# Kernel tuning notes

Hardware: AMD Instinct MI355X
Metric: run time of the kernel (lower is better)

The kernel has to match this reference:

```python
import jax, jax.numpy as jnp
import numpy as np

N = 100000          # num nodes
E = 1600000         # num edges (before self loops)
IN_C = 128
OUT_C = 64
RATIO = 0.5
NEG_SLOPE = 0.2


def setup_inputs() -> dict:
    key = jax.random.key(0)
    k1, k2, k3, k4, k5 = jax.random.split(key, 5)
    x = jax.random.normal(k1, (N, IN_C), jnp.float32)
    # edges with no self loops (module removes then re-adds self loops)
    src = jax.random.randint(k2, (E,), 0, N, dtype=jnp.int32)
    off = jax.random.randint(k3, (E,), 1, N, dtype=jnp.int32)
    tgt = (src + off) % N
    edge_index = jnp.stack([src, tgt])  # [2, E], row0=source(j), row1=target(i)
    # glorot init
    s_w = float(np.sqrt(6.0 / (IN_C + OUT_C)))
    weight = jax.random.uniform(k4, (IN_C, OUT_C), jnp.float32, -s_w, s_w)
    s_a = float(np.sqrt(6.0 / (1 + 2 * OUT_C)))
    att = jax.random.uniform(k5, (1, 2 * OUT_C), jnp.float32, -s_a, s_a)
    batch = jnp.zeros((N,), jnp.int32)  # single graph
    return {"x": x, "weight": weight, "att": att,
            "edge_index": edge_index, "batch": batch, "bn": 0}


def reference(x, weight, att, edge_index, batch, bn):
    # add self loops (static shapes: E + N edges)
    loops = jnp.arange(N, dtype=edge_index.dtype)
    src = jnp.concatenate([edge_index[0], loops])  # edge_index_j (source)
    tgt = jnp.concatenate([edge_index[1], loops])  # edge_index_i (target)

    h = x @ weight                      # [N, OUT_C]
    x_j = h[src]                        # [E+N, OUT_C] gathered source feats
    x_i = h[tgt]

    # alpha = (cat([x_i, x_j]) * att).sum(-1)
    alpha = x_i @ att[0, :OUT_C] + x_j @ att[0, OUT_C:]   # [E+N]
    alpha = jnp.where(alpha > 0, alpha, NEG_SLOPE * alpha)  # leaky_relu

    # edge-softmax grouped by target node (every node has a self loop -> no empty segment)
    m = jax.ops.segment_max(alpha, tgt, num_segments=N)
    a = jnp.exp(alpha - m[tgt])
    denom = jax.ops.segment_sum(a, tgt, num_segments=N)
    alpha = a / (denom[tgt] + 1e-16)

    # node importance = sum of attention over outgoing edges (grouped by source)
    alpha_sum = jax.ops.segment_sum(alpha, src, num_segments=N)

    # topk node selection (ratio of all nodes; single graph)
    k = int(np.ceil(RATIO * N))
    _, topk_idx = jax.lax.top_k(alpha_sum, k)
    node_mask = jnp.zeros((N,), bool).at[topk_idx].set(True)

    # filter_dn: keep edges whose both endpoints survive; mask instead of compacting
    edge_mask = node_mask[src] & node_mask[tgt]
    alpha_m = jnp.where(edge_mask, alpha, 0.0)

    # weighted scatter-add aggregation to target nodes (aggr='add')
    out = jax.ops.segment_sum(alpha_m[:, None] * x_j, tgt, num_segments=N)  # [N, OUT_C]
    # bn flag is 0 -> BatchNorm skipped
    return out, edge_mask, node_mask
```

## Files before the change

kernel.cpp:

```cpp
#include <hip/hip_runtime.h>
#include <stdint.h>

#define IN_C 128
#define OUT_C 64
#define NEG_SLOPE 0.2f
#define RB 256
#define RBINS 512
#define STAGE 8192
#define NGH (RBINS * RB)
#define NGHS (RBINS * RBINS)
#define KC 8
#define SXW 192

typedef unsigned int u32;
typedef unsigned long long u64;

__device__ __forceinline__ u32 fenc(float f) {
  u32 u = __float_as_uint(f);
  return (u & 0x80000000u) ? ~u : (u | 0x80000000u);
}
__device__ __forceinline__ u64 key64(float v, int i) {
  return (((u64)fenc(v)) << 32) | (u64)(0xffffffffu - (u32)i);
}

__global__ __launch_bounds__(128) void k_gemm(const float* __restrict__ x,
                                              const float* __restrict__ w,
                                              const float* __restrict__ att,
                                              float* __restrict__ h,
                                              float* __restrict__ ai, float* __restrict__ aj,
                                              int N) {
  __shared__ float sw[IN_C * OUT_C];
  __shared__ float sx[KC * SXW];
  int tid = threadIdx.x;
  int rbase = blockIdx.x * 128;

  for (int i = tid; i < (IN_C * OUT_C) / 4; i += 128)
    ((float4*)sw)[i] = ((const float4*)w)[i];

  int c0 = (tid & 7) * 8;
  int rg = tid >> 3;
  int sxbase = rg * 12;
  float acc[8][8];
#pragma unroll
  for (int i = 0; i < 8; i++)
#pragma unroll
    for (int j = 0; j < 8; j++) acc[i][j] = 0.f;

  int grow = rbase + tid;
  int base = (tid >> 3) * 12 + (tid & 7);
  const float* xp = &x[(size_t)grow * IN_C];

  float4 pv0 = make_float4(0.f, 0.f, 0.f, 0.f);
  float4 pv1 = make_float4(0.f, 0.f, 0.f, 0.f);
  if (grow < N) {
    pv0 = *(const float4*)&xp[0];
    pv1 = *(const float4*)&xp[4];
  }

  for (int kb = 0; kb < IN_C; kb += KC) {
    __syncthreads();
    sx[0 * SXW + base] = pv0.x;
    sx[1 * SXW + base] = pv0.y;
    sx[2 * SXW + base] = pv0.z;
    sx[3 * SXW + base] = pv0.w;
    sx[4 * SXW + base] = pv1.x;
    sx[5 * SXW + base] = pv1.y;
    sx[6 * SXW + base] = pv1.z;
    sx[7 * SXW + base] = pv1.w;
    if (kb + KC < IN_C && grow < N) {
      pv0 = *(const float4*)&xp[kb + KC];
      pv1 = *(const float4*)&xp[kb + KC + 4];
    }
    __syncthreads();
#pragma unroll
    for (int kl = 0; kl < KC; ++kl) {
      int kg = kb + kl;
      float xr[8], wv[8];
      *(float4*)&xr[0] = *(const float4*)&sx[kl * SXW + sxbase];
      *(float4*)&xr[4] = *(const float4*)&sx[kl * SXW + sxbase + 4];
      *(float4*)&wv[0] = *(const float4*)&sw[kg * OUT_C + c0];
      *(float4*)&wv[4] = *(const float4*)&sw[kg * OUT_C + c0 + 4];
#pragma unroll
      for (int i = 0; i < 8; ++i)
#pragma unroll
        for (int j = 0; j < 8; ++j)
          acc[i][j] += xr[i] * wv[j];
    }
  }

  float pi[8], pj[8];
#pragma unroll
  for (int i = 0; i < 8; ++i) { pi[i] = 0.f; pj[i] = 0.f; }
#pragma unroll
  for (int j = 0; j < 8; ++j) {
    float a0 = att[c0 + j], a1 = att[OUT_C + c0 + j];
#pragma unroll
    for (int i = 0; i < 8; ++i) {
      pi[i] += acc[i][j] * a0;
      pj[i] += acc[i][j] * a1;
    }
  }
#pragma unroll
  for (int o = 1; o < 8; o <<= 1) {
#pragma unroll
    for (int i = 0; i < 8; ++i) {
      pi[i] += __shfl_xor(pi[i], o);
      pj[i] += __shfl_xor(pj[i], o);
    }
  }
#pragma unroll
  for (int i = 0; i < 8; ++i) {
    int row = rbase + rg * 8 + i;
    if (row < N) {
      *(float4*)&h[(size_t)row * OUT_C + c0]     = make_float4(acc[i][0], acc[i][1], acc[i][2], acc[i][3]);
      *(float4*)&h[(size_t)row * OUT_C + c0 + 4] = make_float4(acc[i][4], acc[i][5], acc[i][6], acc[i][7]);
      if ((tid & 7) == 0) { ai[row] = pi[i]; aj[row] = pj[i]; }
    }
  }
}

__global__ __launch_bounds__(256) void k_rhist_t(const int* __restrict__ tgt,
                                                 int E, int EN, int chunk, u32* __restrict__ gh,
                                                 u32* __restrict__ hist8, u32* __restrict__ done,
                                                 u32* __restrict__ sel, u32* __restrict__ cnt, u32 k) {
  __shared__ u32 lh[RBINS];
  int tid = threadIdx.x, b = blockIdx.x;
  if (b == 0) {
    for (int i = tid; i < 2048; i += 256) hist8[i] = 0u;
    if (tid < 8) { done[tid] = 0u; cnt[tid] = 0u; }
    if (tid == 0) { sel[0] = 0u; sel[1] = 0u; sel[2] = k; sel[3] = 0u; }
  }
  for (int d = tid; d < RBINS; d += 256) lh[d] = 0u;
  __syncthreads();
  int lo = b * chunk, hi = min(lo + chunk, EN);
  for (int e = lo + tid; e < hi; e += 256) {
    int t = (e < E) ? tgt[e] : e - E;
    atomicAdd(&lh[((u32)t) >> 8], 1u);
  }
  __syncthreads();
  for (int d = tid; d < RBINS; d += 256) gh[d * RB + b] = lh[d];
}

__global__ __launch_bounds__(256) void k_scanA(const u32* __restrict__ in, u32* __restrict__ out,
                                               u32* __restrict__ bsum, int n) {
  __shared__ u32 s[256];
  int i = blockIdx.x * 256 + threadIdx.x;
  u32 v = (i < n) ? in[i] : 0u;
  s[threadIdx.x] = v;
  __syncthreads();
  for (int o = 1; o < 256; o <<= 1) {
    u32 t = (threadIdx.x >= (unsigned)o) ? s[threadIdx.x - o] : 0u;
    __syncthreads();
    s[threadIdx.x] += t;
    __syncthreads();
  }
  if (i < n) out[i] = s[threadIdx.x] - v;
  if (threadIdx.x == 255) bsum[blockIdx.x] = s[255];
}

__global__ __launch_bounds__(1024) void k_scanB(u32* __restrict__ bsum, int nb) {
  __shared__ u32 s[1024];
  int tid = threadIdx.x;
  u32 v = (tid < nb) ? bsum[tid] : 0u;
  s[tid] = v;
  __syncthreads();
  for (int o = 1; o < 1024; o <<= 1) {
    u32 t = (tid >= o) ? s[tid - o] : 0u;
    __syncthreads();
    s[tid] += t;
    __syncthreads();
  }
  if (tid < nb) bsum[tid] = s[tid] - v;
}

__global__ __launch_bounds__(256) void k_scanC(u32* __restrict__ out, const u32* __restrict__ bsum, int n) {
  int i = blockIdx.x * 256 + threadIdx.x;
  if (i < n) out[i] += bsum[blockIdx.x];
}

__global__ __launch_bounds__(256) void k_rscatter_t(const int* __restrict__ src, const int* __restrict__ tgt,
                                                    int E, int EN, int chunk,
                                                    const u32* __restrict__ gh, u32* __restrict__ bufB) {
  __shared__ u32 cnt[RBINS];
  int tid = threadIdx.x, b = blockIdx.x;
  for (int d = tid; d < RBINS; d += 256) cnt[d] = gh[d * RB + b];
  __syncthreads();
  int lo = b * chunk, hi = min(lo + chunk, EN);
  for (int e = lo + tid; e < hi; e += 256) {
    int s, t;
    if (e < E) { s = src[e]; t = tgt[e]; } else { s = t = e - E; }
    u32 p = atomicAdd(&cnt[((u32)t) >> 8], 1u);
    bufB[p] = (((u32)t & 255u) << 24) | (u32)s;
  }
}

__global__ __launch_bounds__(256) void k_rpass2(const u32* __restrict__ in, u32* __restrict__ out,
                                                const u32* __restrict__ gh, u32* __restrict__ ghs,
                                                u32* __restrict__ offT,
                                                const float* __restrict__ ai, const float* __restrict__ aj,
                                                float* __restrict__ alpha,
                                                int N, int EN) {
  __shared__ u32 hist[256];
  __shared__ u32 sc[256];
  __shared__ u32 lhs[RBINS];
  __shared__ u32 stage[STAGE];
  int tid = threadIdx.x, d = blockIdx.x;
  u32 start = gh[d * RB];
  u32 end = (d < RBINS - 1) ? gh[(d + 1) * RB] : (u32)EN;
  int sz = (int)(end - start);
  hist[tid] = 0u;
  for (int dd = tid; dd < RBINS; dd += 256) lhs[dd] = 0u;
  __syncthreads();
  for (u32 p = start + tid; p < end; p += 256) {
    u32 it = in[p];
    atomicAdd(&hist[it >> 24], 1u);
    atomicAdd(&lhs[(it & 0xffffffu) >> 8], 1u);
  }
  __syncthreads();
  for (int dd = tid; dd < RBINS; dd += 256) ghs[dd * RBINS + d] = lhs[dd];
  u32 hv = hist[tid];
  sc[tid] = hv;
  __syncthreads();
  for (int o = 1; o < 256; o <<= 1) {
    u32 t = (tid >= o) ? sc[tid - o] : 0u;
    __syncthreads();
    sc[tid] += t;
    __syncthreads();
  }
  u32 excl = sc[tid] - hv;
  int node = (d << 8) + tid;
  if (node < N) offT[node] = start + excl;
  if (node == 0) offT[N] = (u32)EN;
  hist[tid] = excl;
  __syncthreads();
  bool staged = (sz <= STAGE);
  for (u32 p = start + tid; p < end; p += 256) {
    u32 it = in[p];
    u32 lp = atomicAdd(&hist[it >> 24], 1u);
    if (staged) stage[lp] = it;
    else out[start + lp] = it;
  }
  __syncthreads();
  if (staged)
    for (int i = tid; i < sz; i += 256) out[start + i] = stage[i];
  __syncthreads();
  if (node < N) {
    int lb = (tid > 0) ? (int)sc[tid - 1] : 0;
    int le = (int)sc[tid];
    float an = ai[node];
    float mx = -1e30f;
    for (int i = lb; i < le; ++i) {
      u32 it = staged ? stage[i] : out[start + i];
      float a = an + aj[it & 0xffffffu];
      a = a > 0.f ? a : NEG_SLOPE * a;
      mx = fmaxf(mx, a);
      if (staged) stage[i] = __float_as_uint(a);
    }
    float sm = 0.f;
    for (int i = lb; i < le; ++i) {
      float a;
      if (staged) a = __uint_as_float(stage[i]);
      else {
        u32 it = out[start + i];
        a = an + aj[it & 0xffffffu];
        a = a > 0.f ? a : NEG_SLOPE * a;
      }
      float v = expf(a - mx);
      sm += v;
      if (staged) stage[i] = __float_as_uint(v);
      else alpha[start + i] = v;
    }
    float inv = 1.f / (sm + 1e-16f);
    for (int i = lb; i < le; ++i) {
      float v = staged ? __uint_as_float(stage[i]) : alpha[start + i];
      alpha[start + i] = v * inv;
    }
  }
}

__global__ __launch_bounds__(256) void k_rscatter_s(const u32* __restrict__ csr,
                                                    const float* __restrict__ alpha,
                                                    const u32* __restrict__ gh, const u32* __restrict__ ghs,
                                                    u64* __restrict__ bufB, int EN) {
  __shared__ u32 cnt[RBINS];
  int tid = threadIdx.x, d = blockIdx.x;
  for (int dd = tid; dd < RBINS; dd += 256) cnt[dd] = ghs[dd * RBINS + d];
  __syncthreads();
  u32 start = gh[d * RB];
  u32 end = (d < RBINS - 1) ? gh[(d + 1) * RB] : (u32)EN;
  for (u32 e = start + tid; e < end; e += 256) {
    u32 s = csr[e] & 0xffffffu;
    u32 p = atomicAdd(&cnt[s >> 8], 1u);
    bufB[p] = (((u64)(s & 255u)) << 32) | __float_as_uint(alpha[e]);
  }
}

__global__ __launch_bounds__(256) void k_asum_acc(const u64* __restrict__ bufB,
                                                  const u32* __restrict__ ghs,
                                                  float* __restrict__ asum,
                                                  u32* __restrict__ hist8, u32* __restrict__ done,
                                                  u32* __restrict__ sel,
                                                  int N, int EN, int nblk) {
  __shared__ float sums[256];
  __shared__ u32 lh[256];
  __shared__ u32 s[256];
  __shared__ u32 sres;
  int tid = threadIdx.x, d = blockIdx.x;
  u32 start = ghs[d * RBINS];
  u32 end = (d < RBINS - 1) ? ghs[(d + 1) * RBINS] : (u32)EN;
  sums[tid] = 0.f;
  __syncthreads();
  for (u32 p = start + tid; p < end; p += 256) {
    u64 it = bufB[p];
    atomicAdd(&sums[(u32)(it >> 32)], __uint_as_float((u32)it));
  }
  __syncthreads();
  int node = d * 256 + tid;
  u32 bin = 256u;
  if (node < N) {
    float v = sums[tid];
    asum[node] = v;
    bin = (u32)(key64(v, node) >> 56) & 255u;
  }
  lh[tid] = 0u;
  __syncthreads();
  if (bin < 256u) atomicAdd(&lh[bin], 1u);
  __syncthreads();
  if (lh[tid]) atomicAdd(&hist8[tid], lh[tid]);
  __syncthreads();
  if (tid == 0)
    sres = __hip_atomic_fetch_add(&done[0], 1u, __ATOMIC_ACQ_REL, __HIP_MEMORY_SCOPE_AGENT);
  __syncthreads();
  if (sres == (u32)(nblk - 1)) {
    u32 krem = sel[2];
    u32 hv = __hip_atomic_load(&hist8[255 - tid], __ATOMIC_RELAXED, __HIP_MEMORY_SCOPE_AGENT);
    s[tid] = hv;
    __syncthreads();
    for (int o = 1; o < 256; o <<= 1) {
      u32 t = (tid >= o) ? s[tid - o] : 0u;
      __syncthreads();
      s[tid] += t;
      __syncthreads();
    }
    u32 cum = s[tid], prev = (tid > 0) ? s[tid - 1] : 0u;
    if (cum >= krem && prev < krem) {
      int dsel = 255 - tid;
      ((u64*)sel)[0] = (u64)(u32)dsel;
      sel[2] = krem - prev;
    }
  }
}

__global__ __launch_bounds__(256) void k_histpick(const float* __restrict__ asum,
                                                  const u32* __restrict__ list_in, const u32* __restrict__ cnt_in,
                                                  u32* __restrict__ list_out, u32* __restrict__ cnt_out,
                                                  u32* __restrict__ hist8, u32* __restrict__ done,
                                                  u32* __restrict__ sel, int N, int pass, int nblk) {
  __shared__ u32 lh[256];
  __shared__ u32 sres;
  __shared__ u32 s[256];
  int tid = threadIdx.x;
  lh[tid] = 0u;
  __syncthreads();
  u64 prefix = ((const u64*)sel)[0];
  int shift = 56 - 8 * pass;
  int n = list_in ? (int)*cnt_in : N;
  int i = blockIdx.x * 256 + tid;
  if (i < n) {
    int idx = list_in ? (int)list_in[i] : i;
    u64 k = key64(asum[idx], idx);
    bool ok = (pass == 0) || ((k >> (shift + 8)) == prefix);
    if (ok) {
      atomicAdd(&lh[(u32)(k >> shift) & 255u], 1u);
      if (list_out) {
        u32 p = atomicAdd(cnt_out, 1u);
        list_out[p] = (u32)idx;
      }
    }
  }
  __syncthreads();
  if (lh[tid]) atomicAdd(&hist8[pass * 256 + tid], lh[tid]);
  __syncthreads();
  if (tid == 0)
    sres = __hip_atomic_fetch_add(&done[pass], 1u, __ATOMIC_ACQ_REL, __HIP_MEMORY_SCOPE_AGENT);
  __syncthreads();
  if (sres == (u32)(nblk - 1)) {
    u32 krem = sel[2];
    u32 hv = __hip_atomic_load(&hist8[pass * 256 + (255 - tid)], __ATOMIC_RELAXED,
                               __HIP_MEMORY_SCOPE_AGENT);
    s[tid] = hv;
    __syncthreads();
    for (int o = 1; o < 256; o <<= 1) {
      u32 t = (tid >= o) ? s[tid - o] : 0u;
      __syncthreads();
      s[tid] += t;
      __syncthreads();
    }
    u32 cum = s[tid], prev = (tid > 0) ? s[tid - 1] : 0u;
    if (cum >= krem && prev < krem) {
      int dsel = 255 - tid;
      ((u64*)sel)[0] = (prefix << 8) | (u64)(u32)dsel;
      sel[2] = krem - prev;
    }
  }
}

__global__ __launch_bounds__(256) void k_finish(const float* __restrict__ asum,
                                                const u32* __restrict__ list, const u32* __restrict__ cntp,
                                                u32* __restrict__ sel) {
  __shared__ u64 keys[2048];
  __shared__ u32 cc;
  int tid = threadIdx.x;
  if (tid == 0) cc = 0u;
  __syncthreads();
  int n = (int)*cntp;
  u32 fsel = (u32)((const u64*)sel)[0];
  u32 krem = sel[2];
  for (int i = tid; i < n; i += 256) {
    int idx = (int)list[i];
    u64 k = key64(asum[idx], idx);
    if ((u32)(k >> 32) == fsel) {
      u32 p = atomicAdd(&cc, 1u);
      if (p < 2048) keys[p] = k;
    }
  }
  __syncthreads();
  int C = (int)min(cc, 2048u);
  for (int i = tid; i < C; i += 256) {
    u64 k = keys[i];
    u32 rank = 0;
    for (int j = 0; j < C; ++j)
      if (keys[j] > k) rank++;
    if (rank == krem - 1) ((u64*)sel)[0] = k;
  }
}

__global__ __launch_bounds__(256) void k_node_mask(const float* __restrict__ asum,
                                                   const u32* __restrict__ sel,
                                                   u32* __restrict__ nm,
                                                   float* __restrict__ out_node, int N) {
  int i = blockIdx.x * 256 + threadIdx.x;
  if (i >= N) return;
  u64 T = ((const u64*)sel)[0];
  bool m = key64(asum[i], i) >= T;
  nm[i] = m ? 1u : 0u;
  out_node[i] = m ? 1.f : 0.f;
}

__global__ __launch_bounds__(256) void k_mask(const int* __restrict__ src, const int* __restrict__ tgt,
                                              const u32* __restrict__ nm,
                                              float* __restrict__ out_edge,
                                              int E, int EN) {
  int e = blockIdx.x * 256 + threadIdx.x;
  if (e >= EN) return;
  int s, t;
  if (e < E) { s = src[e]; t = tgt[e]; } else { s = t = e - E; }
  out_edge[e] = (nm[s] && nm[t]) ? 1.f : 0.f;
}

__global__ __launch_bounds__(256) void k_aggregate(const u32* __restrict__ off,
                                                   const u32* __restrict__ csr,
                                                   const float* __restrict__ alpha,
                                                   const float* __restrict__ h,
                                                   const u32* __restrict__ nm,
                                                   float* __restrict__ out, int N) {
  int node = blockIdx.x * 4 + (threadIdx.x >> 6);
  int lane = threadIdx.x & 63;
  int g = lane >> 4;
  int c = lane & 15;
  if (node >= N) return;
  float4 acc = make_float4(0.f, 0.f, 0.f, 0.f);
  if (nm[node]) {
    u32 b = off[node], e2 = off[node + 1];
    for (u32 p0 = b; p0 < e2; p0 += 16) {
      float av[4];
      u32 sv[4];
#pragma unroll
      for (int q = 0; q < 4; ++q) {
        u32 p = p0 + q * 4 + (u32)g;
        bool ok = p < e2;
        u32 pp = ok ? p : b;
        u32 sp = csr[pp] & 0xffffffu;
        float a = alpha[pp];
        sv[q] = sp;
        av[q] = (ok && nm[sp]) ? a : 0.f;
      }
      float4 hv[4];
#pragma unroll
      for (int q = 0; q < 4; ++q) {
        hv[q] = make_float4(0.f, 0.f, 0.f, 0.f);
        if (av[q] != 0.f)
          hv[q] = *(const float4*)&h[(size_t)sv[q] * OUT_C + c * 4];
      }
#pragma unroll
      for (int q = 0; q < 4; ++q) {
        acc.x += av[q] * hv[q].x;
        acc.y += av[q] * hv[q].y;
        acc.z += av[q] * hv[q].z;
        acc.w += av[q] * hv[q].w;
      }
    }
#pragma unroll
    for (int o = 16; o < 64; o <<= 1) {
      acc.x += __shfl_xor(acc.x, o);
      acc.y += __shfl_xor(acc.y, o);
      acc.z += __shfl_xor(acc.z, o);
      acc.w += __shfl_xor(acc.w, o);
    }
  }
  if (g == 0)
    *(float4*)&out[(size_t)node * OUT_C + c * 4] = acc;
}

extern "C" void kernel_launch(void* const* d_in, const int* in_sizes, int n_in,
                              void* d_out, int out_size, void* d_ws, size_t ws_size,
                              hipStream_t stream) {
  const float* x   = (const float*)d_in[0];
  const float* w   = (const float*)d_in[1];
  const float* att = (const float*)d_in[2];
  const int*   ei  = (const int*)d_in[3];

  int N = in_sizes[0] / IN_C;
  int E = in_sizes[3] / 2;
  int EN = E + N;
  const int* src = ei;
  const int* tgt = ei + E;

  float* out      = (float*)d_out;
  float* out_edge = out + (size_t)N * OUT_C;
  float* out_node = out_edge + (size_t)EN;

  char* p = (char*)d_ws;
  auto alloc = [&](size_t bytes) -> char* {
    char* r = p;
    p += (bytes + 255) & ~(size_t)255;
    return r;
  };
  float* h     = (float*)alloc((size_t)N * OUT_C * 4);
  float* ai    = (float*)alloc((size_t)N * 4);
  float* aj    = (float*)alloc((size_t)N * 4);
  u32*   bufA  = (u32*)alloc((size_t)EN * 4);
  u64*   bufB  = (u64*)alloc((size_t)EN * 8);
  float* alpha = (float*)alloc((size_t)EN * 4);
  u32*   offT  = (u32*)alloc((size_t)(N + 1) * 4);
  u32*   gh    = (u32*)alloc((size_t)NGH * 4);
  u32*   ghs   = (u32*)alloc((size_t)NGHS * 4);
  u32*   bsum  = (u32*)alloc(2048 * 4);
  float* asum  = (float*)alloc((size_t)N * 4);
  u32*   nm    = (u32*)alloc((size_t)N * 4);
  u32*   hist8 = (u32*)alloc(2048 * 4);
  u32*   done  = (u32*)alloc(8 * 4);
  u32*   cnt   = (u32*)alloc(8 * 4);
  u32*   sel   = (u32*)alloc(256);
  u32*   listA = (u32*)alloc((size_t)N * 4);
  u32*   listB = (u32*)alloc((size_t)N * 4);

  u32 kSel = (u32)((N + 1) / 2);
  int chunk = (EN + RB - 1) / RB;
  int nScanT = (NGH + 255) / 256;
  int nScanS = (NGHS + 255) / 256;
  int gGemm = (N + 127) / 128;
  int gN = (N + 255) / 256;
  int gE = (EN + 255) / 256;
  int gNode4 = (N + 3) / 4;

  k_gemm<<<gGemm, 128, 0, stream>>>(x, w, att, h, ai, aj, N);

  k_rhist_t<<<RB, 256, 0, stream>>>(tgt, E, EN, chunk, gh, hist8, done, sel, cnt, kSel);
  k_scanA<<<nScanT, 256, 0, stream>>>(gh, gh, bsum, NGH);
  k_scanB<<<1, 1024, 0, stream>>>(bsum, nScanT);
  k_scanC<<<nScanT, 256, 0, stream>>>(gh, bsum, NGH);
  k_rscatter_t<<<RB, 256, 0, stream>>>(src, tgt, E, EN, chunk, gh, (u32*)bufB);
  k_rpass2<<<RBINS, 256, 0, stream>>>((u32*)bufB, bufA, gh, ghs, offT, ai, aj, alpha, N, EN);

  k_scanA<<<nScanS, 256, 0, stream>>>(ghs, ghs, bsum, NGHS);
  k_scanB<<<1, 1024, 0, stream>>>(bsum, nScanS);
  k_scanC<<<nScanS, 256, 0, stream>>>(ghs, bsum, NGHS);
  k_rscatter_s<<<RBINS, 256, 0, stream>>>(bufA, alpha, gh, ghs, bufB, EN);
  k_asum_acc<<<RBINS, 256, 0, stream>>>(bufB, ghs, asum, hist8, done, sel, N, EN, RBINS);

  k_histpick<<<gN, 256, 0, stream>>>(asum, nullptr, nullptr, listA, &cnt[1],
                                     hist8, done, sel, N, 1, gN);
  k_histpick<<<gN, 256, 0, stream>>>(asum, listA, &cnt[1], listB, &cnt[2],
                                     hist8, done, sel, N, 2, gN);
  k_histpick<<<gN, 256, 0, stream>>>(asum, listB, &cnt[2], listA, &cnt[3],
                                     hist8, done, sel, N, 3, gN);
  k_finish<<<1, 256, 0, stream>>>(asum, listA, &cnt[3], sel);

  k_node_mask<<<gN, 256, 0, stream>>>(asum, sel, nm, out_node, N);
  k_mask<<<gE, 256, 0, stream>>>(src, tgt, nm, out_edge, E, EN);
  k_aggregate<<<gNode4, 256, 0, stream>>>(offT, bufA, alpha, h, nm, out, N);
}
```

Measured before the change: 362.4 us.

## Replace scan-based radix partitions with fixed-capacity bucket slots and fewer top-k passes

```diff
diff --git a/kernel.cpp b/kernel.cpp
--- a/kernel.cpp
+++ b/kernel.cpp
@@ -7,12 +7,13 @@
 #define RB 256
 #define RBINS 512
 #define STAGE 8192
-#define NGH (RBINS * RB)
-#define NGHS (RBINS * RBINS)
+#define SCAP 5120
+#define SGRID (RBINS * SCAP)
 #define KC 8
 #define SXW 192
 
 typedef unsigned int u32;
+typedef unsigned char u8;
 typedef unsigned long long u64;
 
 __device__ __forceinline__ u32 fenc(float f) {
@@ -119,17 +120,14 @@
   }
 }
 
-__global__ __launch_bounds__(256) void k_rhist_t(const int* __restrict__ tgt,
-                                                 int E, int EN, int chunk, u32* __restrict__ gh,
-                                                 u32* __restrict__ hist8, u32* __restrict__ done,
-                                                 u32* __restrict__ sel, u32* __restrict__ cnt, u32 k) {
+__global__ __launch_bounds__(256) void k_part_t(const int* __restrict__ src, const int* __restrict__ tgt,
+                                                int E, int EN, int chunk,
+                                                u32* __restrict__ gcurT, u32* __restrict__ bufS,
+                                                u32* __restrict__ sel, u32 kSel) {
   __shared__ u32 lh[RBINS];
+  __shared__ u32 cur[RBINS];
   int tid = threadIdx.x, b = blockIdx.x;
-  if (b == 0) {
-    for (int i = tid; i < 2048; i += 256) hist8[i] = 0u;
-    if (tid < 8) { done[tid] = 0u; cnt[tid] = 0u; }
-    if (tid == 0) { sel[0] = 0u; sel[1] = 0u; sel[2] = k; sel[3] = 0u; }
-  }
+  if (b == 0 && tid == 0) { sel[0] = 0u; sel[1] = 0u; sel[2] = kSel; sel[3] = 0u; }
   for (int d = tid; d < RBINS; d += 256) lh[d] = 0u;
   __syncthreads();
   int lo = b * chunk, hi = min(lo + chunk, EN);
@@ -138,76 +136,36 @@
     atomicAdd(&lh[((u32)t) >> 8], 1u);
   }
   __syncthreads();
-  for (int d = tid; d < RBINS; d += 256) gh[d * RB + b] = lh[d];
-}
-
-__global__ __launch_bounds__(256) void k_scanA(const u32* __restrict__ in, u32* __restrict__ out,
-                                               u32* __restrict__ bsum, int n) {
-  __shared__ u32 s[256];
-  int i = blockIdx.x * 256 + threadIdx.x;
-  u32 v = (i < n) ? in[i] : 0u;
-  s[threadIdx.x] = v;
-  __syncthreads();
-  for (int o = 1; o < 256; o <<= 1) {
-    u32 t = (threadIdx.x >= (unsigned)o) ? s[threadIdx.x - o] : 0u;
-    __syncthreads();
-    s[threadIdx.x] += t;
-    __syncthreads();
-  }
-  if (i < n) out[i] = s[threadIdx.x] - v;
-  if (threadIdx.x == 255) bsum[blockIdx.x] = s[255];
-}
-
-__global__ __launch_bounds__(1024) void k_scanB(u32* __restrict__ bsum, int nb) {
-  __shared__ u32 s[1024];
-  int tid = threadIdx.x;
-  u32 v = (tid < nb) ? bsum[tid] : 0u;
-  s[tid] = v;
-  __syncthreads();
-  for (int o = 1; o < 1024; o <<= 1) {
-    u32 t = (tid >= o) ? s[tid - o] : 0u;
-    __syncthreads();
-    s[tid] += t;
-    __syncthreads();
-  }
-  if (tid < nb) bsum[tid] = s[tid] - v;
-}
-
-__global__ __launch_bounds__(256) void k_scanC(u32* __restrict__ out, const u32* __restrict__ bsum, int n) {
-  int i = blockIdx.x * 256 + threadIdx.x;
-  if (i < n) out[i] += bsum[blockIdx.x];
-}
-
-__global__ __launch_bounds__(256) void k_rscatter_t(const int* __restrict__ src, const int* __restrict__ tgt,
-                                                    int E, int EN, int chunk,
-                                                    const u32* __restrict__ gh, u32* __restrict__ bufB) {
-  __shared__ u32 cnt[RBINS];
-  int tid = threadIdx.x, b = blockIdx.x;
-  for (int d = tid; d < RBINS; d += 256) cnt[d] = gh[d * RB + b];
-  __syncthreads();
-  int lo = b * chunk, hi = min(lo + chunk, EN);
+  for (int d = tid; d < RBINS; d += 256) {
+    u32 c = lh[d];
+    cur[d] = c ? (u32)(d * SCAP) + atomicAdd(&gcurT[d], c) : 0u;
+  }
+  __syncthreads();
   for (int e = lo + tid; e < hi; e += 256) {
     int s, t;
     if (e < E) { s = src[e]; t = tgt[e]; } else { s = t = e - E; }
-    u32 p = atomicAdd(&cnt[((u32)t) >> 8], 1u);
-    bufB[p] = (((u32)t & 255u) << 24) | (u32)s;
+    u32 tb = ((u32)t) >> 8;
+    u32 p = atomicAdd(&cur[tb], 1u);
+    if (p < (tb + 1u) * SCAP) bufS[p] = (((u32)t & 255u) << 24) | (u32)s;
   }
 }
 
 __global__ __launch_bounds__(256) void k_rpass2(const u32* __restrict__ in, u32* __restrict__ out,
-                                                const u32* __restrict__ gh, u32* __restrict__ ghs,
+                                                const u32* __restrict__ gcurT, u32* __restrict__ gcurS,
                                                 u32* __restrict__ offT,
                                                 const float* __restrict__ ai, const float* __restrict__ aj,
                                                 float* __restrict__ alpha,
-                                                int N, int EN) {
+                                                u8* __restrict__ pidx, float* __restrict__ pval,
+                                                int N) {
   __shared__ u32 hist[256];
   __shared__ u32 sc[256];
   __shared__ u32 lhs[RBINS];
   __shared__ u32 stage[STAGE];
   int tid = threadIdx.x, d = blockIdx.x;
-  u32 start = gh[d * RB];
-  u32 end = (d < RBINS - 1) ? gh[(d + 1) * RB] : (u32)EN;
-  int sz = (int)(end - start);
+  u32 start = (u32)(d * SCAP);
+  u32 cntb = min(gcurT[d], (u32)SCAP);
+  u32 end = start + cntb;
+  int sz = (int)cntb;
   hist[tid] = 0u;
   for (int dd = tid; dd < RBINS; dd += 256) lhs[dd] = 0u;
   __syncthreads();
@@ -217,7 +175,10 @@
     atomicAdd(&lhs[(it & 0xffffffu) >> 8], 1u);
   }
   __syncthreads();
-  for (int dd = tid; dd < RBINS; dd += 256) ghs[dd * RBINS + d] = lhs[dd];
+  for (int dd = tid; dd < RBINS; dd += 256) {
+    u32 c = lhs[dd];
+    lhs[dd] = c ? (u32)(dd * SCAP) + atomicAdd(&gcurS[dd], c) : 0u;
+  }
   u32 hv = hist[tid];
   sc[tid] = hv;
   __syncthreads();
@@ -230,7 +191,7 @@
   u32 excl = sc[tid] - hv;
   int node = (d << 8) + tid;
   if (node < N) offT[node] = start + excl;
-  if (node == 0) offT[N] = (u32)EN;
+  if (node == N - 1) offT[N] = start + sc[tid];
   hist[tid] = excl;
   __syncthreads();
   bool staged = (sz <= STAGE);
@@ -276,44 +237,35 @@
       alpha[start + i] = v * inv;
     }
   }
-}
-
-__global__ __launch_bounds__(256) void k_rscatter_s(const u32* __restrict__ csr,
-                                                    const float* __restrict__ alpha,
-                                                    const u32* __restrict__ gh, const u32* __restrict__ ghs,
-                                                    u64* __restrict__ bufB, int EN) {
-  __shared__ u32 cnt[RBINS];
-  int tid = threadIdx.x, d = blockIdx.x;
-  for (int dd = tid; dd < RBINS; dd += 256) cnt[dd] = ghs[dd * RBINS + d];
-  __syncthreads();
-  u32 start = gh[d * RB];
-  u32 end = (d < RBINS - 1) ? gh[(d + 1) * RB] : (u32)EN;
-  for (u32 e = start + tid; e < end; e += 256) {
-    u32 s = csr[e] & 0xffffffu;
-    u32 p = atomicAdd(&cnt[s >> 8], 1u);
-    bufB[p] = (((u64)(s & 255u)) << 32) | __float_as_uint(alpha[e]);
-  }
-}
-
-__global__ __launch_bounds__(256) void k_asum_acc(const u64* __restrict__ bufB,
-                                                  const u32* __restrict__ ghs,
+  __syncthreads();
+  for (u32 p = start + tid; p < end; p += 256) {
+    u32 sp = out[p] & 0xffffffu;
+    u32 sb = sp >> 8;
+    u32 pos = atomicAdd(&lhs[sb], 1u);
+    if (pos < (sb + 1u) * SCAP) {
+      pidx[pos] = (u8)(sp & 255u);
+      pval[pos] = alpha[p];
+    }
+  }
+}
+
+__global__ __launch_bounds__(256) void k_asum_acc(const u8* __restrict__ pidx,
+                                                  const float* __restrict__ pval,
+                                                  const u32* __restrict__ gcurS,
                                                   float* __restrict__ asum,
                                                   u32* __restrict__ hist8, u32* __restrict__ done,
-                                                  u32* __restrict__ sel,
-                                                  int N, int EN, int nblk) {
+                                                  u32* __restrict__ sel, int N, int nblk) {
   __shared__ float sums[256];
   __shared__ u32 lh[256];
   __shared__ u32 s[256];
   __shared__ u32 sres;
   int tid = threadIdx.x, d = blockIdx.x;
-  u32 start = ghs[d * RBINS];
-  u32 end = (d < RBINS - 1) ? ghs[(d + 1) * RBINS] : (u32)EN;
+  u32 start = (u32)(d * SCAP);
+  u32 end = start + min(gcurS[d], (u32)SCAP);
   sums[tid] = 0.f;
   __syncthreads();
-  for (u32 p = start + tid; p < end; p += 256) {
-    u64 it = bufB[p];
-    atomicAdd(&sums[(u32)(it >> 32)], __uint_as_float((u32)it));
-  }
+  for (u32 p = start + tid; p < end; p += 256)
+    atomicAdd(&sums[pidx[p]], pval[p]);
   __syncthreads();
   int node = d * 256 + tid;
   u32 bin = 256u;
@@ -344,18 +296,16 @@
     }
     u32 cum = s[tid], prev = (tid > 0) ? s[tid - 1] : 0u;
     if (cum >= krem && prev < krem) {
-      int dsel = 255 - tid;
-      ((u64*)sel)[0] = (u64)(u32)dsel;
+      ((u64*)sel)[0] = (u64)(u32)(255 - tid);
       sel[2] = krem - prev;
     }
   }
 }
 
 __global__ __launch_bounds__(256) void k_histpick(const float* __restrict__ asum,
-                                                  const u32* __restrict__ list_in, const u32* __restrict__ cnt_in,
                                                   u32* __restrict__ list_out, u32* __restrict__ cnt_out,
                                                   u32* __restrict__ hist8, u32* __restrict__ done,
-                                                  u32* __restrict__ sel, int N, int pass, int nblk) {
+                                                  u32* __restrict__ sel, int N, int nblk) {
   __shared__ u32 lh[256];
   __shared__ u32 sres;
   __shared__ u32 s[256];
@@ -363,30 +313,24 @@
   lh[tid] = 0u;
   __syncthreads();
   u64 prefix = ((const u64*)sel)[0];
-  int shift = 56 - 8 * pass;
-  int n = list_in ? (int)*cnt_in : N;
   int i = blockIdx.x * 256 + tid;
-  if (i < n) {
-    int idx = list_in ? (int)list_in[i] : i;
-    u64 k = key64(asum[idx], idx);
-    bool ok = (pass == 0) || ((k >> (shift + 8)) == prefix);
-    if (ok) {
-      atomicAdd(&lh[(u32)(k >> shift) & 255u], 1u);
-      if (list_out) {
-        u32 p = atomicAdd(cnt_out, 1u);
-        list_out[p] = (u32)idx;
-      }
-    }
-  }
-  __syncthreads();
-  if (lh[tid]) atomicAdd(&hist8[pass * 256 + tid], lh[tid]);
+  if (i < N) {
+    u64 k = key64(asum[i], i);
+    if ((k >> 56) == prefix) {
+      atomicAdd(&lh[(u32)(k >> 48) & 255u], 1u);
+      u32 p = atomicAdd(cnt_out, 1u);
+      list_out[p] = (u32)i;
+    }
+  }
+  __syncthreads();
+  if (lh[tid]) atomicAdd(&hist8[256 + tid], lh[tid]);
   __syncthreads();
   if (tid == 0)
-    sres = __hip_atomic_fetch_add(&done[pass], 1u, __ATOMIC_ACQ_REL, __HIP_MEMORY_SCOPE_AGENT);
+    sres = __hip_atomic_fetch_add(&done[1], 1u, __ATOMIC_ACQ_REL, __HIP_MEMORY_SCOPE_AGENT);
   __syncthreads();
   if (sres == (u32)(nblk - 1)) {
     u32 krem = sel[2];
-    u32 hv = __hip_atomic_load(&hist8[pass * 256 + (255 - tid)], __ATOMIC_RELAXED,
+    u32 hv = __hip_atomic_load(&hist8[256 + (255 - tid)], __ATOMIC_RELAXED,
                                __HIP_MEMORY_SCOPE_AGENT);
     s[tid] = hv;
     __syncthreads();
@@ -398,26 +342,90 @@
     }
     u32 cum = s[tid], prev = (tid > 0) ? s[tid - 1] : 0u;
     if (cum >= krem && prev < krem) {
-      int dsel = 255 - tid;
-      ((u64*)sel)[0] = (prefix << 8) | (u64)(u32)dsel;
+      ((u64*)sel)[0] = (prefix << 8) | (u64)(u32)(255 - tid);
       sel[2] = krem - prev;
     }
   }
 }
 
-__global__ __launch_bounds__(256) void k_finish(const float* __restrict__ asum,
-                                                const u32* __restrict__ list, const u32* __restrict__ cntp,
-                                                u32* __restrict__ sel) {
+__global__ __launch_bounds__(256) void k_histpick_final(const float* __restrict__ asum,
+                                                        const u32* __restrict__ list_in, const u32* __restrict__ cnt_in,
+                                                        u32* __restrict__ list_out, u32* __restrict__ cnt_out,
+                                                        u32* __restrict__ hist8, u32* __restrict__ done,
+                                                        u32* __restrict__ sel, int nblk) {
+  __shared__ u32 lh[256];
+  __shared__ u32 s[256];
+  __shared__ u32 sres;
   __shared__ u64 keys[2048];
   __shared__ u32 cc;
+  __shared__ u64 sprefix;
+  __shared__ u32 skrem;
   int tid = threadIdx.x;
+  lh[tid] = 0u;
+  __syncthreads();
+  u64 prefix = ((const u64*)sel)[0];
+  u32 n = *cnt_in;
+  u32 i = blockIdx.x * 256 + tid;
+  if (i < n) {
+    int idx = (int)list_in[i];
+    u64 k = key64(asum[idx], idx);
+    if ((k >> 48) == prefix) {
+      atomicAdd(&lh[(u32)(k >> 40) & 255u], 1u);
+      u32 p = atomicAdd(cnt_out, 1u);
+      list_out[p] = (u32)idx;
+    }
+  }
+  __syncthreads();
+  if (lh[tid]) atomicAdd(&hist8[512 + tid], lh[tid]);
+  __syncthreads();
+  if (tid == 0)
+    sres = __hip_atomic_fetch_add(&done[2], 1u, __ATOMIC_ACQ_REL, __HIP_MEMORY_SCOPE_AGENT);
+  __syncthreads();
+  if (sres != (u32)(nblk - 1)) return;
+  u32 krem = sel[2];
+  u32 hv = __hip_atomic_load(&hist8[512 + (255 - tid)], __ATOMIC_RELAXED, __HIP_MEMORY_SCOPE_AGENT);
+  s[tid] = hv;
+  __syncthreads();
+  for (int o = 1; o < 256; o <<= 1) {
+    u32 t = (tid >= o) ? s[tid - o] : 0u;
+    __syncthreads();
+    s[tid] += t;
+    __syncthreads();
+  }
+  {
+    u32 cum = s[tid], prev = (tid > 0) ? s[tid - 1] : 0u;
+    if (cum >= krem && prev < krem) { sprefix = (prefix << 8) | (u64)(u32)(255 - tid); skrem = krem - prev; }
+  }
+  __syncthreads();
+  u64 pfx3 = sprefix;
+  u32 krem3 = skrem;
+  u32 n3 = *cnt_out;
+  lh[tid] = 0u;
+  __syncthreads();
+  for (u32 j = tid; j < n3; j += 256) {
+    int idx = (int)list_out[j];
+    u64 k = key64(asum[idx], idx);
+    if ((k >> 40) == pfx3) atomicAdd(&lh[(u32)(k >> 32) & 255u], 1u);
+  }
+  __syncthreads();
+  s[tid] = lh[255 - tid];
+  __syncthreads();
+  for (int o = 1; o < 256; o <<= 1) {
+    u32 t = (tid >= o) ? s[tid - o] : 0u;
+    __syncthreads();
+    s[tid] += t;
+    __syncthreads();
+  }
+  {
+    u32 cum = s[tid], prev = (tid > 0) ? s[tid - 1] : 0u;
+    if (cum >= krem3 && prev < krem3) { sprefix = (pfx3 << 8) | (u64)(u32)(255 - tid); skrem = krem3 - prev; }
+  }
   if (tid == 0) cc = 0u;
   __syncthreads();
-  int n = (int)*cntp;
-  u32 fsel = (u32)((const u64*)sel)[0];
-  u32 krem = sel[2];
-  for (int i = tid; i < n; i += 256) {
-    int idx = (int)list[i];
+  u32 fsel = (u32)sprefix;
+  u32 kremF = skrem;
+  for (u32 j = tid; j < n3; j += 256) {
+    int idx = (int)list_out[j];
     u64 k = key64(asum[idx], idx);
     if ((u32)(k >> 32) == fsel) {
       u32 p = atomicAdd(&cc, 1u);
@@ -426,12 +434,12 @@
   }
   __syncthreads();
   int C = (int)min(cc, 2048u);
-  for (int i = tid; i < C; i += 256) {
-    u64 k = keys[i];
+  for (int j = tid; j < C; j += 256) {
+    u64 k = keys[j];
     u32 rank = 0;
-    for (int j = 0; j < C; ++j)
-      if (keys[j] > k) rank++;
-    if (rank == krem - 1) ((u64*)sel)[0] = k;
+    for (int q = 0; q < C; ++q)
+      if (keys[q] > k) rank++;
+    if (rank == kremF - 1) ((u64*)sel)[0] = k;
   }
 }
 
@@ -449,13 +457,25 @@
 
 __global__ __launch_bounds__(256) void k_mask(const int* __restrict__ src, const int* __restrict__ tgt,
                                               const u32* __restrict__ nm,
-                                              float* __restrict__ out_edge,
-                                              int E, int EN) {
-  int e = blockIdx.x * 256 + threadIdx.x;
-  if (e >= EN) return;
-  int s, t;
-  if (e < E) { s = src[e]; t = tgt[e]; } else { s = t = e - E; }
-  out_edge[e] = (nm[s] && nm[t]) ? 1.f : 0.f;
+                                              const u32* __restrict__ csr, float* __restrict__ alpha,
+                                              const u32* __restrict__ gcurT,
+                                              float* __restrict__ out_edge, int E, int EN) {
+  int q = blockIdx.x * 256 + threadIdx.x;
+  if (q < EN) {
+    int s, t;
+    if (q < E) { s = src[q]; t = tgt[q]; } else { s = t = q - E; }
+    out_edge[q] = (nm[s] && nm[t]) ? 1.f : 0.f;
+  }
+  if (q < SGRID) {
+    u32 b = (u32)q / (u32)SCAP;
+    u32 r = (u32)q - b * (u32)SCAP;
+    float a = 0.f;
+    if (r < min(gcurT[b], (u32)SCAP)) {
+      u32 sp = csr[q] & 0xffffffu;
+      if (nm[sp]) a = alpha[q];
+    }
+    alpha[q] = a;
+  }
 }
 
 __global__ __launch_bounds__(256) void k_aggregate(const u32* __restrict__ off,
@@ -472,28 +492,27 @@
   float4 acc = make_float4(0.f, 0.f, 0.f, 0.f);
   if (nm[node]) {
     u32 b = off[node], e2 = off[node + 1];
-    for (u32 p0 = b; p0 < e2; p0 += 16) {
-      float av[4];
-      u32 sv[4];
-#pragma unroll
-      for (int q = 0; q < 4; ++q) {
+    for (u32 p0 = b; p0 < e2; p0 += 32) {
+      float av[8];
+      u32 sv[8];
+#pragma unroll
+      for (int q = 0; q < 8; ++q) {
         u32 p = p0 + q * 4 + (u32)g;
         bool ok = p < e2;
         u32 pp = ok ? p : b;
-        u32 sp = csr[pp] & 0xffffffu;
+        sv[q] = csr[pp] & 0xffffffu;
         float a = alpha[pp];
-        sv[q] = sp;
-        av[q] = (ok && nm[sp]) ? a : 0.f;
+        av[q] = ok ? a : 0.f;
       }
-      float4 hv[4];
-#pragma unroll
-      for (int q = 0; q < 4; ++q) {
+      float4 hv[8];
+#pragma unroll
+      for (int q = 0; q < 8; ++q) {
         hv[q] = make_float4(0.f, 0.f, 0.f, 0.f);
         if (av[q] != 0.f)
           hv[q] = *(const float4*)&h[(size_t)sv[q] * OUT_C + c * 4];
       }
 #pragma unroll
-      for (int q = 0; q < 4; ++q) {
+      for (int q = 0; q < 8; ++q) {
         acc.x += av[q] * hv[q].x;
         acc.y += av[q] * hv[q].y;
         acc.z += av[q] * hv[q].z;
@@ -539,55 +558,46 @@
   float* h     = (float*)alloc((size_t)N * OUT_C * 4);
   float* ai    = (float*)alloc((size_t)N * 4);
   float* aj    = (float*)alloc((size_t)N * 4);
-  u32*   bufA  = (u32*)alloc((size_t)EN * 4);
-  u64*   bufB  = (u64*)alloc((size_t)EN * 8);
-  float* alpha = (float*)alloc((size_t)EN * 4);
+  u32*   bufA  = (u32*)alloc((size_t)SGRID * 4);
+  u32*   stg   = (u32*)alloc((size_t)SGRID * 4);
+  u8*    pidx  = (u8*)alloc((size_t)SGRID);
+  float* pval  = (float*)alloc((size_t)SGRID * 4);
   u32*   offT  = (u32*)alloc((size_t)(N + 1) * 4);
-  u32*   gh    = (u32*)alloc((size_t)NGH * 4);
-  u32*   ghs   = (u32*)alloc((size_t)NGHS * 4);
-  u32*   bsum  = (u32*)alloc(2048 * 4);
   float* asum  = (float*)alloc((size_t)N * 4);
   u32*   nm    = (u32*)alloc((size_t)N * 4);
-  u32*   hist8 = (u32*)alloc(2048 * 4);
-  u32*   done  = (u32*)alloc(8 * 4);
-  u32*   cnt   = (u32*)alloc(8 * 4);
-  u32*   sel   = (u32*)alloc(256);
   u32*   listA = (u32*)alloc((size_t)N * 4);
   u32*   listB = (u32*)alloc((size_t)N * 4);
+  u32*   zb    = (u32*)alloc((RBINS + RBINS + 2048 + 8 + 8) * 4);
+  u32*   gcurT = zb;
+  u32*   gcurS = zb + RBINS;
+  u32*   hist8 = zb + 2 * RBINS;
+  u32*   done  = zb + 2 * RBINS + 2048;
+  u32*   cnt   = zb + 2 * RBINS + 2048 + 8;
+  u32*   sel   = (u32*)alloc(256);
+
+  float* alpha = (float*)stg;
 
   u32 kSel = (u32)((N + 1) / 2);
   int chunk = (EN + RB - 1) / RB;
-  int nScanT = (NGH + 255) / 256;
-  int nScanS = (NGHS + 255) / 256;
   int gGemm = (N + 127) / 128;
   int gN = (N + 255) / 256;
-  int gE = (EN + 255) / 256;
+  int gS = (SGRID + 255) / 256;
   int gNode4 = (N + 3) / 4;
 
+  hipMemsetAsync(zb, 0, (RBINS + RBINS + 2048 + 8 + 8) * 4, stream);
+
   k_gemm<<<gGemm, 128, 0, stream>>>(x, w, att, h, ai, aj, N);
 
-  k_rhist_t<<<RB, 256, 0, stream>>>(tgt, E, EN, chunk, gh, hist8, done, sel, cnt, kSel);
-  k_scanA<<<nScanT, 256, 0, stream>>>(gh, gh, bsum, NGH);
-  k_scanB<<<1, 1024, 0, stream>>>(bsum, nScanT);
-  k_scanC<<<nScanT, 256, 0, stream>>>(gh, bsum, NGH);
-  k_rscatter_t<<<RB, 256, 0, stream>>>(src, tgt, E, EN, chunk, gh, (u32*)bufB);
-  k_rpass2<<<RBINS, 256, 0, stream>>>((u32*)bufB, bufA, gh, ghs, offT, ai, aj, alpha, N, EN);
-
-  k_scanA<<<nScanS, 256, 0, stream>>>(ghs, ghs, bsum, NGHS);
-  k_scanB<<<1, 1024, 0, stream>>>(bsum, nScanS);
-  k_scanC<<<nScanS, 256, 0, stream>>>(ghs, bsum, NGHS);
-  k_rscatter_s<<<RBINS, 256, 0, stream>>>(bufA, alpha, gh, ghs, bufB, EN);
-  k_asum_acc<<<RBINS, 256, 0, stream>>>(bufB, ghs, asum, hist8, done, sel, N, EN, RBINS);
-
-  k_histpick<<<gN, 256, 0, stream>>>(asum, nullptr, nullptr, listA, &cnt[1],
-                                     hist8, done, sel, N, 1, gN);
-  k_histpick<<<gN, 256, 0, stream>>>(asum, listA, &cnt[1], listB, &cnt[2],
-                                     hist8, done, sel, N, 2, gN);
-  k_histpick<<<gN, 256, 0, stream>>>(asum, listB, &cnt[2], listA, &cnt[3],
-                                     hist8, done, sel, N, 3, gN);
-  k_finish<<<1, 256, 0, stream>>>(asum, listA, &cnt[3], sel);
+  k_part_t<<<RB, 256, 0, stream>>>(src, tgt, E, EN, chunk, gcurT, stg, sel, kSel);
+  k_rpass2<<<RBINS, 256, 0, stream>>>(stg, bufA, gcurT, gcurS, offT, ai, aj,
+                                      alpha, pidx, pval, N);
+  k_asum_acc<<<RBINS, 256, 0, stream>>>(pidx, pval, gcurS, asum, hist8, done, sel, N, RBINS);
+
+  k_histpick<<<gN, 256, 0, stream>>>(asum, listA, &cnt[1], hist8, done, sel, N, gN);
+  k_histpick_final<<<gN, 256, 0, stream>>>(asum, listA, &cnt[1], listB, &cnt[2],
+                                           hist8, done, sel, gN);
 
   k_node_mask<<<gN, 256, 0, stream>>>(asum, sel, nm, out_node, N);
-  k_mask<<<gE, 256, 0, stream>>>(src, tgt, nm, out_edge, E, EN);
+  k_mask<<<gS, 256, 0, stream>>>(src, tgt, nm, bufA, alpha, gcurT, out_edge, E, EN);
   k_aggregate<<<gNode4, 256, 0, stream>>>(offT, bufA, alpha, h, nm, out, N);
 }
```

After: 386.0 us. 1.07x slower.
